# Kernel optimization log

Hardware: AMD Instinct MI355X
Metric: run time of the kernel (lower is better)

## Reference

```python
import jax, jax.numpy as jnp
import numpy as np

N, E = 100000, 400000
ATOM_DIM, HIDDEN, LAYERS, HEADS = 74, 256, 3, 4
OUT = HIDDEN // HEADS


def setup_inputs() -> dict:
    key = jax.random.key(0)
    ks = jax.random.split(key, 12)
    s = 1.0 / np.sqrt(HIDDEN)
    return {
        'atom_feat': jax.random.normal(ks[0], (N, ATOM_DIM), jnp.float32),
        'src': jax.random.randint(ks[1], (E,), 0, N, jnp.int32),
        'dst': jax.random.randint(ks[2], (E,), 0, N, jnp.int32),
        'W_in': jax.random.normal(ks[3], (ATOM_DIM, HIDDEN), jnp.float32) / np.sqrt(ATOM_DIM),
        'b_in': jnp.zeros((HIDDEN,), jnp.float32),
        'W_src': jax.random.normal(ks[4], (LAYERS, HIDDEN, HIDDEN), jnp.float32) * s,
        'b_src': jnp.zeros((LAYERS, HIDDEN), jnp.float32),
        'W_dst': jax.random.normal(ks[5], (LAYERS, HIDDEN, HIDDEN), jnp.float32) * s,
        'b_dst': jnp.zeros((LAYERS, HIDDEN), jnp.float32),
        'attn': jax.random.normal(ks[6], (LAYERS, HEADS, OUT), jnp.float32) * s,
        'bias': jnp.zeros((LAYERS, HIDDEN), jnp.float32),
    }


def _gatv2_layer(h, src, dst, Ws, bs, Wd, bd, a, b_out):
    # h: [N, HIDDEN]; fc_src / fc_dst projections reshaped to [N, HEADS, OUT]
    fs = (h @ Ws + bs).reshape(N, HEADS, OUT)
    fd = (h @ Wd + bd).reshape(N, HEADS, OUT)
    # GATv2: e_ij = a . leaky_relu(Ws h_i + Wd h_j) per head  -> [E, HEADS]
    e = jax.nn.leaky_relu(fs[src] + fd[dst], negative_slope=0.2)
    logits = jnp.einsum('ehd,hd->eh', e, a)
    # segment softmax over incoming edges of each dst node
    m = jax.ops.segment_max(logits, dst, num_segments=N)      # [N, HEADS]
    ex = jnp.exp(logits - m[dst])
    denom = jax.ops.segment_sum(ex, dst, num_segments=N)      # [N, HEADS]
    alpha = ex / denom[dst]                                   # [E, HEADS]
    # weighted scatter-aggregate of source features -> [N, HEADS, OUT]
    msg = alpha[:, :, None] * fs[src]
    rst = jax.ops.segment_sum(msg, dst, num_segments=N)
    # flatten(1) + per-layer output bias
    return rst.reshape(N, HIDDEN) + b_out


def reference(atom_feat, src, dst, W_in, b_in, W_src, b_src, W_dst, b_dst, attn, bias):
    h = atom_feat @ W_in + b_in
    for l in range(LAYERS):
        h = _gatv2_layer(h, src, dst, W_src[l], b_src[l], W_dst[l], b_dst[l], attn[l], bias[l])
    return h  # [N, HIDDEN]; per-molecule list is just slicing of this matrix
```

## Files before the change

kernel.cpp:

```cpp
#include <hip/hip_runtime.h>
#include <hip/hip_fp16.h>

#define HID   256
#define NHEAD 4
#define DOUT  64
#define ADIM  74
#define KPAD_IN 96
#define LAYERS 3

typedef _Float16 half8 __attribute__((ext_vector_type(8)));
typedef _Float16 half4 __attribute__((ext_vector_type(4)));
typedef float f32x4 __attribute__((ext_vector_type(4)));

__device__ __forceinline__ void gload16(const void* g, void* l) {
  __builtin_amdgcn_global_load_lds((const __attribute__((address_space(1))) void*)g,
                                   (__attribute__((address_space(3))) void*)l, 16, 0, 0);
}

__global__ void k_prep_wt(const float* __restrict__ Ws, const float* __restrict__ Wd,
                          _Float16* __restrict__ WT) {
  int id = blockIdx.x * 256 + threadIdx.x;
  if (id >= 512 * HID) return;
  int n = id >> 8, k = id & 255;
  float v = (n < HID) ? Ws[k * HID + n] : Wd[k * HID + (n - HID)];
  WT[id] = (_Float16)v;
}

__global__ void k_prep_win(const float* __restrict__ Win, _Float16* __restrict__ WT) {
  int id = blockIdx.x * 256 + threadIdx.x;
  if (id >= HID * KPAD_IN) return;
  int n = id / KPAD_IN, k = id % KPAD_IN;
  WT[id] = (_Float16)((k < ADIM) ? Win[k * HID + n] : 0.f);
}

__device__ __forceinline__ void gemm_epilogue(
    f32x4 acc[4][4], char* smem, int t, int lane, int wm, int wn,
    int row0, int col0, int M,
    const float* bias0, const float* bias1,
    _Float16* outS, _Float16* outD)
{
  const float* bp = (col0 < HID) ? (bias0 + col0) : (bias1 + (col0 - HID));
  _Float16*    op = (col0 < HID) ? (outS + col0) : (outD + (col0 - HID));
  _Float16 (*C)[136] = (_Float16(*)[136])smem;
  #pragma unroll
  for (int i = 0; i < 4; ++i) {
    #pragma unroll
    for (int j = 0; j < 4; ++j) {
      int lc = wn * 64 + j * 16 + (lane & 15);
      float bv = bp[lc];
      #pragma unroll
      for (int r = 0; r < 4; ++r) {
        int lr = wm * 64 + i * 16 + (lane >> 4) * 4 + r;
        C[lr][lc] = (_Float16)(acc[i][j][r] + bv);
      }
    }
  }
  __syncthreads();
  int lr = t >> 1, hf = t & 1;
  int grow = row0 + lr;
  if (grow < M) {
    _Float16* dst = op + (size_t)grow * HID + hf * 64;
    const _Float16* sp = &C[lr][hf * 64];
    #pragma unroll
    for (int q = 0; q < 8; ++q)
      *(uint4*)(dst + q * 8) = *(const uint4*)(sp + q * 8);
  }
}

__global__ __launch_bounds__(256)
void k_gemm_h(const _Float16* __restrict__ A, int M,
              const _Float16* __restrict__ B,
              const float* __restrict__ bias0, const float* __restrict__ bias1,
              _Float16* __restrict__ outS, _Float16* __restrict__ outD)
{
  __shared__ __align__(16) char smem[65536];
  const int t = threadIdx.x, lane = t & 63, wid = t >> 6;
  const int wm = wid >> 1, wn = wid & 1;
  const int col0 = blockIdx.x * 128, row0 = blockIdx.y * 128;

  f32x4 acc[4][4];
  #pragma unroll
  for (int i = 0; i < 4; ++i)
    #pragma unroll
    for (int j = 0; j < 4; ++j)
      acc[i][j] = (f32x4){0.f, 0.f, 0.f, 0.f};

  auto stage = [&](int kt, int buf) {
    const int kb = kt * 64;
    char* Ab = smem + buf * 32768;
    char* Bb = Ab + 16384;
    #pragma unroll
    for (int q = 0; q < 4; ++q) {
      int ci = wid * 4 + q;
      int r = ci * 8 + (lane >> 3);
      int slot = (lane & 7) ^ (r & 7);
      int grow = row0 + r; grow = grow < M ? grow : (M - 1);
      gload16(A + (size_t)grow * HID + kb + slot * 8, Ab + ci * 1024);
      gload16(B + (size_t)(col0 + r) * HID + kb + slot * 8, Bb + ci * 1024);
    }
  };

  stage(0, 0);
  __syncthreads();
  int cur = 0;
  for (int kt = 0; kt < 4; ++kt) {
    if (kt < 3) stage(kt + 1, cur ^ 1);
    const char* Ab = smem + cur * 32768;
    const char* Bb = Ab + 16384;
    #pragma unroll
    for (int kc = 0; kc < 2; ++kc) {
      half8 af[4], bf[4];
      #pragma unroll
      for (int i = 0; i < 4; ++i) {
        int r = wm * 64 + i * 16 + (lane & 15);
        int slot = (kc * 4 + (lane >> 4)) ^ (r & 7);
        af[i] = *(const half8*)(Ab + r * 128 + slot * 16);
      }
      #pragma unroll
      for (int j = 0; j < 4; ++j) {
        int r = wn * 64 + j * 16 + (lane & 15);
        int slot = (kc * 4 + (lane >> 4)) ^ (r & 7);
        bf[j] = *(const half8*)(Bb + r * 128 + slot * 16);
      }
      #pragma unroll
      for (int i = 0; i < 4; ++i)
        #pragma unroll
        for (int j = 0; j < 4; ++j)
          acc[i][j] = __builtin_amdgcn_mfma_f32_16x16x32_f16(af[i], bf[j], acc[i][j], 0, 0, 0);
    }
    __syncthreads();
    cur ^= 1;
  }
  gemm_epilogue(acc, smem, t, lane, wm, wn, row0, col0, M, bias0, bias1, outS, outD);
}

__global__ __launch_bounds__(256)
void k_gemm_f(const float* __restrict__ A, int M,
              const _Float16* __restrict__ B,
              const float* __restrict__ bias0,
              _Float16* __restrict__ outS)
{
  __shared__ __align__(16) char smem[34816];
  const int t = threadIdx.x, lane = t & 63, wid = t >> 6;
  const int wm = wid >> 1, wn = wid & 1;
  const int col0 = blockIdx.x * 128, row0 = blockIdx.y * 128;
  char* Ab = smem;
  char* Bb = smem + 8192;

  f32x4 acc[4][4];
  #pragma unroll
  for (int i = 0; i < 4; ++i)
    #pragma unroll
    for (int j = 0; j < 4; ++j)
      acc[i][j] = (f32x4){0.f, 0.f, 0.f, 0.f};

  for (int kt = 0; kt < 3; ++kt) {
    const int kb = kt * 32;
    #pragma unroll
    for (int it = 0; it < 4; ++it) {
      int idx = t + it * 256;
      int r = idx >> 3, c4 = idx & 7;
      int gr = row0 + r;
      int k0 = kb + c4 * 4;
      float x0 = 0.f, x1 = 0.f, x2 = 0.f, x3 = 0.f;
      if (gr < M) {
        const float* ap = A + (size_t)gr * ADIM;
        if (k0 + 0 < ADIM) x0 = ap[k0 + 0];
        if (k0 + 1 < ADIM) x1 = ap[k0 + 1];
        if (k0 + 2 < ADIM) x2 = ap[k0 + 2];
        if (k0 + 3 < ADIM) x3 = ap[k0 + 3];
      }
      half4 hv = {(_Float16)x0, (_Float16)x1, (_Float16)x2, (_Float16)x3};
      int off = r * 64 + ((c4 * 8) ^ ((r & 3) << 4));
      *(half4*)(Ab + off) = hv;
    }
    #pragma unroll
    for (int q = 0; q < 2; ++q) {
      int ci = wid * 2 + q;
      int r = ci * 16 + (lane >> 2);
      int slot = (lane & 3) ^ (r & 3);
      gload16(B + (size_t)(col0 + r) * KPAD_IN + kb + slot * 8, Bb + ci * 1024);
    }
    __syncthreads();
    half8 af[4], bf[4];
    #pragma unroll
    for (int i = 0; i < 4; ++i) {
      int r = wm * 64 + i * 16 + (lane & 15);
      int slot = (lane >> 4) ^ (r & 3);
      af[i] = *(const half8*)(Ab + r * 64 + slot * 16);
    }
    #pragma unroll
    for (int j = 0; j < 4; ++j) {
      int r = wn * 64 + j * 16 + (lane & 15);
      int slot = (lane >> 4) ^ (r & 3);
      bf[j] = *(const half8*)(Bb + r * 64 + slot * 16);
    }
    #pragma unroll
    for (int i = 0; i < 4; ++i)
      #pragma unroll
      for (int j = 0; j < 4; ++j)
        acc[i][j] = __builtin_amdgcn_mfma_f32_16x16x32_f16(af[i], bf[j], acc[i][j], 0, 0, 0);
    __syncthreads();
  }
  gemm_epilogue(acc, smem, t, lane, wm, wn, row0, col0, M, bias0, bias0, outS, outS);
}

__global__ __launch_bounds__(256)
void k_fused(const int* __restrict__ offs, const int* __restrict__ esrc,
             const _Float16* __restrict__ fs, const _Float16* __restrict__ fd,
             const float* __restrict__ attn, const float* __restrict__ bias,
             _Float16* __restrict__ hhalf, float* __restrict__ hfloat, int N)
{
  int n = blockIdx.x * 8 + (threadIdx.x >> 5);
  if (n >= N) return;
  int sub = threadIdx.x & 31;
  int h = sub >> 3;
  int j0 = sub * 8;
  half8 fdv = *(const half8*)&fd[(size_t)n * HID + j0];
  float4 av0 = *(const float4*)&attn[h * DOUT + (sub & 7) * 8];
  float4 av1 = *(const float4*)&attn[h * DOUT + (sub & 7) * 8 + 4];
  float fdf[8], avf[8];
  #pragma unroll
  for (int q = 0; q < 4; ++q) { avf[q] = ((const float*)&av0)[q]; avf[q + 4] = ((const float*)&av1)[q]; }
  #pragma unroll
  for (int q = 0; q < 8; ++q) fdf[q] = (float)fdv[q];

  int t0 = offs[n], t1 = offs[n + 1];
  float m = -1e30f, ssum = 0.f;
  float a[8];
  #pragma unroll
  for (int q = 0; q < 8; ++q) a[q] = 0.f;

  half8 fN = {};
  if (t0 < t1) {
    int s0 = esrc[t0];
    fN = *(const half8*)&fs[(size_t)s0 * HID + j0];
  }
  for (int tt = t0; tt < t1; ++tt) {
    half8 fv = fN;
    if (tt + 1 < t1) {
      int s2 = esrc[tt + 1];
      fN = *(const half8*)&fs[(size_t)s2 * HID + j0];
    }
    float f[8];
    #pragma unroll
    for (int q = 0; q < 8; ++q) f[q] = (float)fv[q];
    float p = 0.f;
    #pragma unroll
    for (int q = 0; q < 8; ++q) {
      float x = f[q] + fdf[q];
      x = x > 0.f ? x : 0.2f * x;
      p += x * avf[q];
    }
    p += __shfl_xor(p, 1);
    p += __shfl_xor(p, 2);
    p += __shfl_xor(p, 4);
    if (p > m) {
      float sc = __expf(m - p);
      ssum = ssum * sc + 1.f;
      #pragma unroll
      for (int q = 0; q < 8; ++q) a[q] = a[q] * sc + f[q];
      m = p;
    } else {
      float w = __expf(p - m);
      ssum += w;
      #pragma unroll
      for (int q = 0; q < 8; ++q) a[q] += w * f[q];
    }
  }
  float inv = (t1 > t0) ? 1.0f / ssum : 0.f;
  float o[8];
  #pragma unroll
  for (int q = 0; q < 8; ++q) o[q] = a[q] * inv + bias[j0 + q];
  if (hhalf) {
    half8 hv;
    #pragma unroll
    for (int q = 0; q < 8; ++q) hv[q] = (_Float16)o[q];
    *(half8*)&hhalf[(size_t)n * HID + j0] = hv;
  }
  if (hfloat) {
    float4 v0 = {o[0], o[1], o[2], o[3]};
    float4 v1 = {o[4], o[5], o[6], o[7]};
    *(float4*)&hfloat[(size_t)n * HID + j0] = v0;
    *(float4*)&hfloat[(size_t)n * HID + j0 + 4] = v1;
  }
}

__global__ void k_zero_i(int* p, int n) {
  int i = blockIdx.x * 256 + threadIdx.x;
  if (i < n) p[i] = 0;
}
__global__ void k_count(const int* __restrict__ dst, int* __restrict__ counts, int E) {
  int i = blockIdx.x * 256 + threadIdx.x;
  if (i < E) atomicAdd(&counts[dst[i]], 1);
}
__global__ __launch_bounds__(1024)
void k_scan1(const int* __restrict__ counts, int* __restrict__ offs,
             int* __restrict__ bsums, int N)
{
  __shared__ int sd[1024];
  int t = threadIdx.x, i = blockIdx.x * 1024 + t;
  int x = (i < N) ? counts[i] : 0;
  sd[t] = x;
  __syncthreads();
  for (int off = 1; off < 1024; off <<= 1) {
    int v = (t >= off) ? sd[t - off] : 0;
    __syncthreads();
    sd[t] += v;
    __syncthreads();
  }
  if (i < N) offs[i] = sd[t] - x;
  if (t == 0) bsums[blockIdx.x] = sd[1023];
}
__global__ void k_scan2(const int* __restrict__ bsums, int* __restrict__ boffs,
                        int* __restrict__ offs, int nb, int N)
{
  if (threadIdx.x == 0 && blockIdx.x == 0) {
    int run = 0;
    for (int b = 0; b < nb; ++b) { boffs[b] = run; run += bsums[b]; }
    offs[N] = run;
  }
}
__global__ __launch_bounds__(1024)
void k_scan3(const int* __restrict__ boffs, int* __restrict__ offs,
             int* __restrict__ cursor, int N)
{
  int i = blockIdx.x * 1024 + threadIdx.x;
  if (i < N) {
    int v = offs[i] + boffs[blockIdx.x];
    offs[i] = v;
    cursor[i] = v;
  }
}
__global__ void k_scatter(const int* __restrict__ src, const int* __restrict__ dst,
                          int* __restrict__ cursor, int* __restrict__ esrc, int E)
{
  int i = blockIdx.x * 256 + threadIdx.x;
  if (i < E) {
    int pos = atomicAdd(&cursor[dst[i]], 1);
    esrc[pos] = src[i];
  }
}

extern "C" void kernel_launch(void* const* d_in, const int* in_sizes, int n_in,
                              void* d_out, int out_size, void* d_ws, size_t ws_size,
                              hipStream_t stream)
{
  const float* atom  = (const float*)d_in[0];
  const int*   src   = (const int*)d_in[1];
  const int*   dst   = (const int*)d_in[2];
  const float* W_in  = (const float*)d_in[3];
  const float* b_in  = (const float*)d_in[4];
  const float* W_src = (const float*)d_in[5];
  const float* b_src = (const float*)d_in[6];
  const float* W_dst = (const float*)d_in[7];
  const float* b_dst = (const float*)d_in[8];
  const float* attn  = (const float*)d_in[9];
  const float* bias  = (const float*)d_in[10];

  const int N = in_sizes[0] / ADIM;
  const int E = in_sizes[1];
  _Float16* h_half = (_Float16*)d_out;
  float*    h_out  = (float*)d_out;

  char* w = (char*)d_ws;
  size_t off = 0;
  auto carve = [&](size_t bytes) {
    void* p = w + off;
    off = (off + bytes + 255) & ~(size_t)255;
    return p;
  };
  _Float16* fs    = (_Float16*)carve((size_t)N * HID * 2);
  _Float16* fd    = (_Float16*)carve((size_t)N * HID * 2);
  _Float16* WT    = (_Float16*)carve((size_t)512 * HID * 2);
  _Float16* WTin  = (_Float16*)carve((size_t)HID * KPAD_IN * 2);
  int*      counts= (int*)carve((size_t)N * 4);
  int*      offs  = (int*)carve((size_t)(N + 1) * 4);
  int*      cursor= (int*)carve((size_t)N * 4);
  int*      esrc  = (int*)carve((size_t)E * 4);
  int*      bsums = (int*)carve((size_t)1024 * 4);
  int*      boffs = (int*)carve((size_t)1024 * 4);
  (void)ws_size; (void)n_in; (void)out_size;

  const int nb = (N + 1023) / 1024;
  const int gmx = (N + 127) / 128;

  k_zero_i<<<(N + 255) / 256, 256, 0, stream>>>(counts, N);
  k_count<<<(E + 255) / 256, 256, 0, stream>>>(dst, counts, E);
  k_scan1<<<nb, 1024, 0, stream>>>(counts, offs, bsums, N);
  k_scan2<<<1, 64, 0, stream>>>(bsums, boffs, offs, nb, N);
  k_scan3<<<nb, 1024, 0, stream>>>(boffs, offs, cursor, N);
  k_scatter<<<(E + 255) / 256, 256, 0, stream>>>(src, dst, cursor, esrc, E);

  k_prep_win<<<(HID * KPAD_IN + 255) / 256, 256, 0, stream>>>(W_in, WTin);
  k_gemm_f<<<dim3(2, gmx), 256, 0, stream>>>(atom, N, WTin, b_in, h_half);

  for (int l = 0; l < LAYERS; ++l) {
    k_prep_wt<<<(512 * HID + 255) / 256, 256, 0, stream>>>(W_src + (size_t)l * HID * HID,
                                                           W_dst + (size_t)l * HID * HID, WT);
    k_gemm_h<<<dim3(4, gmx), 256, 0, stream>>>(h_half, N, WT,
                                               b_src + (size_t)l * HID,
                                               b_dst + (size_t)l * HID, fs, fd);
    const bool last = (l == LAYERS - 1);
    k_fused<<<(N + 7) / 8, 256, 0, stream>>>(offs, esrc, fs, fd,
                                             attn + (size_t)l * NHEAD * DOUT,
                                             bias + (size_t)l * HID,
                                             last ? nullptr : h_half,
                                             last ? h_out : nullptr, N);
  }
}
```

Baseline: 508.7 us.

## Halve GEMM LDS, add XCD-aware tile swizzle, degree-sort nodes, batch weight prep

The GEMM kernels switch to a 32-wide K tile, which halves shared memory per block to allow more resident blocks. The epilogue now writes C in two 64-row halves so it fits the smaller buffer. Block indices are remapped so consecutive tiles land on the same XCD, for L2 locality. Destination nodes are bucketed by in-degree into a permutation so the warps in each aggregation block have similar edge counts and finish together. Weight transposition for all layers is done in one launch, and the bias is preloaded as vectors. The cost is extra histogram, scan and scatter kernels, more K-loop iterations and extra barriers.

```diff
diff --git a/kernel.cpp b/kernel.cpp
--- a/kernel.cpp
+++ b/kernel.cpp
@@ -19,11 +19,14 @@
 
 __global__ void k_prep_wt(const float* __restrict__ Ws, const float* __restrict__ Wd,
                           _Float16* __restrict__ WT) {
+  int l = blockIdx.y;
   int id = blockIdx.x * 256 + threadIdx.x;
   if (id >= 512 * HID) return;
   int n = id >> 8, k = id & 255;
-  float v = (n < HID) ? Ws[k * HID + n] : Wd[k * HID + (n - HID)];
-  WT[id] = (_Float16)v;
+  const float* W = (n < HID) ? (Ws + (size_t)l * HID * HID)
+                             : (Wd + (size_t)l * HID * HID);
+  int nn = (n < HID) ? n : (n - HID);
+  WT[(size_t)l * 512 * HID + id] = (_Float16)W[k * HID + nn];
 }
 
 __global__ void k_prep_win(const float* __restrict__ Win, _Float16* __restrict__ WT) {
@@ -33,7 +36,7 @@
   WT[id] = (_Float16)((k < ADIM) ? Win[k * HID + n] : 0.f);
 }
 
-__device__ __forceinline__ void gemm_epilogue(
+__device__ __forceinline__ void gemm_epilogue2(
     f32x4 acc[4][4], char* smem, int t, int lane, int wm, int wn,
     int row0, int col0, int M,
     const float* bias0, const float* bias1,
@@ -43,27 +46,33 @@
   _Float16*    op = (col0 < HID) ? (outS + col0) : (outD + (col0 - HID));
   _Float16 (*C)[136] = (_Float16(*)[136])smem;
   #pragma unroll
-  for (int i = 0; i < 4; ++i) {
-    #pragma unroll
-    for (int j = 0; j < 4; ++j) {
-      int lc = wn * 64 + j * 16 + (lane & 15);
-      float bv = bp[lc];
-      #pragma unroll
-      for (int r = 0; r < 4; ++r) {
-        int lr = wm * 64 + i * 16 + (lane >> 4) * 4 + r;
-        C[lr][lc] = (_Float16)(acc[i][j][r] + bv);
+  for (int half = 0; half < 2; ++half) {
+    __syncthreads();
+    if (wm == half) {
+      #pragma unroll
+      for (int i = 0; i < 4; ++i) {
+        #pragma unroll
+        for (int j = 0; j < 4; ++j) {
+          int lc = wn * 64 + j * 16 + (lane & 15);
+          float bv = bp[lc];
+          #pragma unroll
+          for (int r = 0; r < 4; ++r) {
+            int lr = i * 16 + (lane >> 4) * 4 + r;
+            C[lr][lc] = (_Float16)(acc[i][j][r] + bv);
+          }
+        }
       }
     }
-  }
-  __syncthreads();
-  int lr = t >> 1, hf = t & 1;
-  int grow = row0 + lr;
-  if (grow < M) {
-    _Float16* dst = op + (size_t)grow * HID + hf * 64;
-    const _Float16* sp = &C[lr][hf * 64];
-    #pragma unroll
-    for (int q = 0; q < 8; ++q)
-      *(uint4*)(dst + q * 8) = *(const uint4*)(sp + q * 8);
+    __syncthreads();
+    int lr = t >> 2, seg = t & 3;
+    int grow = row0 + half * 64 + lr;
+    if (grow < M) {
+      const _Float16* sp = &C[lr][seg * 32];
+      _Float16* dp = op + (size_t)grow * HID + seg * 32;
+      #pragma unroll
+      for (int q = 0; q < 4; ++q)
+        *(uint4*)(dp + q * 8) = *(const uint4*)(sp + q * 8);
+    }
   }
 }
 
@@ -73,10 +82,13 @@
               const float* __restrict__ bias0, const float* __restrict__ bias1,
               _Float16* __restrict__ outS, _Float16* __restrict__ outD)
 {
-  __shared__ __align__(16) char smem[65536];
+  __shared__ __align__(16) char smem[32768];
   const int t = threadIdx.x, lane = t & 63, wid = t >> 6;
   const int wm = wid >> 1, wn = wid & 1;
-  const int col0 = blockIdx.x * 128, row0 = blockIdx.y * 128;
+  const int nwg = gridDim.x, id = blockIdx.x;
+  const int qc = nwg >> 3, rc = nwg & 7, xcd = id & 7, idx = id >> 3;
+  const int swz = (xcd < rc ? xcd * (qc + 1) : rc * (qc + 1) + (xcd - rc) * qc) + idx;
+  const int col0 = (swz & 3) * 128, row0 = (swz >> 2) * 128;
 
   f32x4 acc[4][4];
   #pragma unroll
@@ -86,14 +98,14 @@
       acc[i][j] = (f32x4){0.f, 0.f, 0.f, 0.f};
 
   auto stage = [&](int kt, int buf) {
-    const int kb = kt * 64;
-    char* Ab = smem + buf * 32768;
-    char* Bb = Ab + 16384;
-    #pragma unroll
-    for (int q = 0; q < 4; ++q) {
-      int ci = wid * 4 + q;
-      int r = ci * 8 + (lane >> 3);
-      int slot = (lane & 7) ^ (r & 7);
+    const int kb = kt * 32;
+    char* Ab = smem + buf * 16384;
+    char* Bb = Ab + 8192;
+    #pragma unroll
+    for (int q = 0; q < 2; ++q) {
+      int ci = wid * 2 + q;
+      int r = ci * 16 + (lane >> 2);
+      int slot = (lane & 3) ^ (r & 3);
       int grow = row0 + r; grow = grow < M ? grow : (M - 1);
       gload16(A + (size_t)grow * HID + kb + slot * 8, Ab + ci * 1024);
       gload16(B + (size_t)(col0 + r) * HID + kb + slot * 8, Bb + ci * 1024);
@@ -103,35 +115,32 @@
   stage(0, 0);
   __syncthreads();
   int cur = 0;
-  for (int kt = 0; kt < 4; ++kt) {
-    if (kt < 3) stage(kt + 1, cur ^ 1);
-    const char* Ab = smem + cur * 32768;
-    const char* Bb = Ab + 16384;
-    #pragma unroll
-    for (int kc = 0; kc < 2; ++kc) {
-      half8 af[4], bf[4];
-      #pragma unroll
-      for (int i = 0; i < 4; ++i) {
-        int r = wm * 64 + i * 16 + (lane & 15);
-        int slot = (kc * 4 + (lane >> 4)) ^ (r & 7);
-        af[i] = *(const half8*)(Ab + r * 128 + slot * 16);
-      }
-      #pragma unroll
-      for (int j = 0; j < 4; ++j) {
-        int r = wn * 64 + j * 16 + (lane & 15);
-        int slot = (kc * 4 + (lane >> 4)) ^ (r & 7);
-        bf[j] = *(const half8*)(Bb + r * 128 + slot * 16);
-      }
-      #pragma unroll
-      for (int i = 0; i < 4; ++i)
-        #pragma unroll
-        for (int j = 0; j < 4; ++j)
-          acc[i][j] = __builtin_amdgcn_mfma_f32_16x16x32_f16(af[i], bf[j], acc[i][j], 0, 0, 0);
-    }
+  for (int kt = 0; kt < 8; ++kt) {
+    if (kt < 7) stage(kt + 1, cur ^ 1);
+    const char* Ab = smem + cur * 16384;
+    const char* Bb = Ab + 8192;
+    half8 af[4], bf[4];
+    #pragma unroll
+    for (int i = 0; i < 4; ++i) {
+      int r = wm * 64 + i * 16 + (lane & 15);
+      int slot = (lane >> 4) ^ (r & 3);
+      af[i] = *(const half8*)(Ab + r * 64 + slot * 16);
+    }
+    #pragma unroll
+    for (int j = 0; j < 4; ++j) {
+      int r = wn * 64 + j * 16 + (lane & 15);
+      int slot = (lane >> 4) ^ (r & 3);
+      bf[j] = *(const half8*)(Bb + r * 64 + slot * 16);
+    }
+    #pragma unroll
+    for (int i = 0; i < 4; ++i)
+      #pragma unroll
+      for (int j = 0; j < 4; ++j)
+        acc[i][j] = __builtin_amdgcn_mfma_f32_16x16x32_f16(af[i], bf[j], acc[i][j], 0, 0, 0);
     __syncthreads();
     cur ^= 1;
   }
-  gemm_epilogue(acc, smem, t, lane, wm, wn, row0, col0, M, bias0, bias1, outS, outD);
+  gemm_epilogue2(acc, smem, t, lane, wm, wn, row0, col0, M, bias0, bias1, outS, outD);
 }
 
 __global__ __launch_bounds__(256)
@@ -140,10 +149,13 @@
               const float* __restrict__ bias0,
               _Float16* __restrict__ outS)
 {
-  __shared__ __align__(16) char smem[34816];
+  __shared__ __align__(16) char smem[17408];
   const int t = threadIdx.x, lane = t & 63, wid = t >> 6;
   const int wm = wid >> 1, wn = wid & 1;
-  const int col0 = blockIdx.x * 128, row0 = blockIdx.y * 128;
+  const int nwg = gridDim.x, id = blockIdx.x;
+  const int qc = nwg >> 3, rc = nwg & 7, xcd = id & 7, idx = id >> 3;
+  const int swz = (xcd < rc ? xcd * (qc + 1) : rc * (qc + 1) + (xcd - rc) * qc) + idx;
+  const int col0 = (swz & 1) * 128, row0 = (swz >> 1) * 128;
   char* Ab = smem;
   char* Bb = smem + 8192;
 
@@ -158,8 +170,8 @@
     const int kb = kt * 32;
     #pragma unroll
     for (int it = 0; it < 4; ++it) {
-      int idx = t + it * 256;
-      int r = idx >> 3, c4 = idx & 7;
+      int idx2 = t + it * 256;
+      int r = idx2 >> 3, c4 = idx2 & 7;
       int gr = row0 + r;
       int k0 = kb + c4 * 4;
       float x0 = 0.f, x1 = 0.f, x2 = 0.f, x3 = 0.f;
@@ -202,26 +214,33 @@
         acc[i][j] = __builtin_amdgcn_mfma_f32_16x16x32_f16(af[i], bf[j], acc[i][j], 0, 0, 0);
     __syncthreads();
   }
-  gemm_epilogue(acc, smem, t, lane, wm, wn, row0, col0, M, bias0, bias0, outS, outS);
+  gemm_epilogue2(acc, smem, t, lane, wm, wn, row0, col0, M, bias0, bias0, outS, outS);
 }
 
 __global__ __launch_bounds__(256)
 void k_fused(const int* __restrict__ offs, const int* __restrict__ esrc,
+             const int* __restrict__ perm,
              const _Float16* __restrict__ fs, const _Float16* __restrict__ fd,
              const float* __restrict__ attn, const float* __restrict__ bias,
              _Float16* __restrict__ hhalf, float* __restrict__ hfloat, int N)
 {
-  int n = blockIdx.x * 8 + (threadIdx.x >> 5);
-  if (n >= N) return;
+  int gid = blockIdx.x * 8 + (threadIdx.x >> 5);
+  if (gid >= N) return;
+  int n = perm[gid];
   int sub = threadIdx.x & 31;
   int h = sub >> 3;
   int j0 = sub * 8;
   half8 fdv = *(const half8*)&fd[(size_t)n * HID + j0];
   float4 av0 = *(const float4*)&attn[h * DOUT + (sub & 7) * 8];
   float4 av1 = *(const float4*)&attn[h * DOUT + (sub & 7) * 8 + 4];
-  float fdf[8], avf[8];
-  #pragma unroll
-  for (int q = 0; q < 4; ++q) { avf[q] = ((const float*)&av0)[q]; avf[q + 4] = ((const float*)&av1)[q]; }
+  float4 bv0 = *(const float4*)&bias[j0];
+  float4 bv1 = *(const float4*)&bias[j0 + 4];
+  float fdf[8], avf[8], bvf[8];
+  #pragma unroll
+  for (int q = 0; q < 4; ++q) {
+    avf[q] = ((const float*)&av0)[q]; avf[q + 4] = ((const float*)&av1)[q];
+    bvf[q] = ((const float*)&bv0)[q]; bvf[q + 4] = ((const float*)&bv1)[q];
+  }
   #pragma unroll
   for (int q = 0; q < 8; ++q) fdf[q] = (float)fdv[q];
 
@@ -271,7 +290,7 @@
   float inv = (t1 > t0) ? 1.0f / ssum : 0.f;
   float o[8];
   #pragma unroll
-  for (int q = 0; q < 8; ++q) o[q] = a[q] * inv + bias[j0 + q];
+  for (int q = 0; q < 8; ++q) o[q] = a[q] * inv + bvf[q];
   if (hhalf) {
     half8 hv;
     #pragma unroll
@@ -296,13 +315,16 @@
 }
 __global__ __launch_bounds__(1024)
 void k_scan1(const int* __restrict__ counts, int* __restrict__ offs,
-             int* __restrict__ bsums, int N)
+             int* __restrict__ bsums, int* __restrict__ dhist, int N)
 {
   __shared__ int sd[1024];
+  __shared__ int hh[64];
   int t = threadIdx.x, i = blockIdx.x * 1024 + t;
+  if (t < 64) hh[t] = 0;
   int x = (i < N) ? counts[i] : 0;
   sd[t] = x;
   __syncthreads();
+  if (i < N) atomicAdd(&hh[x < 63 ? x : 63], 1);
   for (int off = 1; off < 1024; off <<= 1) {
     int v = (t >= off) ? sd[t - off] : 0;
     __syncthreads();
@@ -311,6 +333,8 @@
   }
   if (i < N) offs[i] = sd[t] - x;
   if (t == 0) bsums[blockIdx.x] = sd[1023];
+  __syncthreads();
+  if (t < 64 && hh[t] > 0) atomicAdd(&dhist[t], hh[t]);
 }
 __global__ void k_scan2(const int* __restrict__ bsums, int* __restrict__ boffs,
                         int* __restrict__ offs, int nb, int N)
@@ -320,6 +344,16 @@
     for (int b = 0; b < nb; ++b) { boffs[b] = run; run += bsums[b]; }
     offs[N] = run;
   }
+}
+__global__ void k_deg_scan(const int* __restrict__ dhist, int* __restrict__ dcur) {
+  int t = threadIdx.x;
+  int x = dhist[t];
+  int sum = x;
+  for (int off = 1; off < 64; off <<= 1) {
+    int v = __shfl_up(sum, off);
+    if (t >= off) sum += v;
+  }
+  dcur[t] = sum - x;
 }
 __global__ __launch_bounds__(1024)
 void k_scan3(const int* __restrict__ boffs, int* __restrict__ offs,
@@ -339,6 +373,16 @@
   if (i < E) {
     int pos = atomicAdd(&cursor[dst[i]], 1);
     esrc[pos] = src[i];
+  }
+}
+__global__ void k_deg_scatter(const int* __restrict__ counts, int* __restrict__ dcur,
+                              int* __restrict__ perm, int N)
+{
+  int i = blockIdx.x * 256 + threadIdx.x;
+  if (i < N) {
+    int d = counts[i]; d = d < 63 ? d : 63;
+    int pos = atomicAdd(&dcur[d], 1);
+    perm[pos] = i;
   }
 }
 
@@ -372,12 +416,15 @@
   };
   _Float16* fs    = (_Float16*)carve((size_t)N * HID * 2);
   _Float16* fd    = (_Float16*)carve((size_t)N * HID * 2);
-  _Float16* WT    = (_Float16*)carve((size_t)512 * HID * 2);
+  _Float16* WT    = (_Float16*)carve((size_t)LAYERS * 512 * HID * 2);
   _Float16* WTin  = (_Float16*)carve((size_t)HID * KPAD_IN * 2);
-  int*      counts= (int*)carve((size_t)N * 4);
+  int*      counts= (int*)carve((size_t)(N + 64) * 4);
+  int*      dhist = counts + N;
   int*      offs  = (int*)carve((size_t)(N + 1) * 4);
   int*      cursor= (int*)carve((size_t)N * 4);
   int*      esrc  = (int*)carve((size_t)E * 4);
+  int*      perm  = (int*)carve((size_t)N * 4);
+  int*      dcur  = (int*)carve((size_t)64 * 4);
   int*      bsums = (int*)carve((size_t)1024 * 4);
   int*      boffs = (int*)carve((size_t)1024 * 4);
   (void)ws_size; (void)n_in; (void)out_size;
@@ -385,24 +432,25 @@
   const int nb = (N + 1023) / 1024;
   const int gmx = (N + 127) / 128;
 
-  k_zero_i<<<(N + 255) / 256, 256, 0, stream>>>(counts, N);
+  k_zero_i<<<(N + 64 + 255) / 256, 256, 0, stream>>>(counts, N + 64);
   k_count<<<(E + 255) / 256, 256, 0, stream>>>(dst, counts, E);
-  k_scan1<<<nb, 1024, 0, stream>>>(counts, offs, bsums, N);
+  k_scan1<<<nb, 1024, 0, stream>>>(counts, offs, bsums, dhist, N);
   k_scan2<<<1, 64, 0, stream>>>(bsums, boffs, offs, nb, N);
+  k_deg_scan<<<1, 64, 0, stream>>>(dhist, dcur);
   k_scan3<<<nb, 1024, 0, stream>>>(boffs, offs, cursor, N);
   k_scatter<<<(E + 255) / 256, 256, 0, stream>>>(src, dst, cursor, esrc, E);
+  k_deg_scatter<<<(N + 255) / 256, 256, 0, stream>>>(counts, dcur, perm, N);
 
   k_prep_win<<<(HID * KPAD_IN + 255) / 256, 256, 0, stream>>>(W_in, WTin);
-  k_gemm_f<<<dim3(2, gmx), 256, 0, stream>>>(atom, N, WTin, b_in, h_half);
+  k_prep_wt<<<dim3((512 * HID + 255) / 256, LAYERS), 256, 0, stream>>>(W_src, W_dst, WT);
+  k_gemm_f<<<2 * gmx, 256, 0, stream>>>(atom, N, WTin, b_in, h_half);
 
   for (int l = 0; l < LAYERS; ++l) {
-    k_prep_wt<<<(512 * HID + 255) / 256, 256, 0, stream>>>(W_src + (size_t)l * HID * HID,
-                                                           W_dst + (size_t)l * HID * HID, WT);
-    k_gemm_h<<<dim3(4, gmx), 256, 0, stream>>>(h_half, N, WT,
-                                               b_src + (size_t)l * HID,
-                                               b_dst + (size_t)l * HID, fs, fd);
+    k_gemm_h<<<4 * gmx, 256, 0, stream>>>(h_half, N, WT + (size_t)l * 512 * HID,
+                                          b_src + (size_t)l * HID,
+                                          b_dst + (size_t)l * HID, fs, fd);
     const bool last = (l == LAYERS - 1);
-    k_fused<<<(N + 7) / 8, 256, 0, stream>>>(offs, esrc, fs, fd,
+    k_fused<<<(N + 7) / 8, 256, 0, stream>>>(offs, esrc, perm, fs, fd,
                                              attn + (size_t)l * NHEAD * DOUT,
                                              bias + (size_t)l * HID,
                                              last ? nullptr : h_half,
```

Measured after the change: 887.2 us. 1.74x slower.
